# Optimization experiments

Measured on AMD Instinct MI355X. Metric: run time of the kernel, lower is better.

The kernel has to match this reference:

```python
import jax, jax.numpy as jnp
import numpy as np

B, N, C, H, NC = 8, 4096, 512, 256, 1000
GRID = 64  # N = GRID*GRID unique positions
LN_EPS = 1e-5


def setup_inputs() -> dict:
    key = jax.random.key(0)
    ks = jax.random.split(key, 10)
    # unique integer grid positions, same for every batch element (original order)
    i = jnp.arange(N)
    base = jnp.stack([i % GRID, i // GRID], axis=-1).astype(jnp.float32)  # [N,2]
    pos_org = jnp.broadcast_to(base, (B, N, 2))
    # per-batch random permutation -> shuffled positions (as the backbone would emit)
    perm = jax.vmap(lambda k: jax.random.permutation(k, N))(jax.random.split(ks[0], B))  # [B,N]
    pos_shuffled = jnp.take_along_axis(pos_org, perm[..., None], axis=1)
    s = 0.02
    return {
        "feat": jax.random.normal(ks[1], (B, N, C), jnp.float32),
        "prev_out": jax.random.normal(ks[2], (B, N, C), jnp.float32),
        "pos_org": pos_org,
        "pos_shuffled": pos_shuffled,
        "proj_W": jax.random.normal(ks[3], (C, C), jnp.float32) * s,
        "proj_b": jnp.zeros((C,), jnp.float32),
        "ln_g": jnp.ones((C,), jnp.float32),
        "ln_b": jnp.zeros((C,), jnp.float32),
        "W1": jax.random.normal(ks[4], (H, C), jnp.float32) * s,
        "b1": jnp.zeros((H,), jnp.float32),
        "W2": jax.random.normal(ks[5], (H, H), jnp.float32) * s,
        "b2": jnp.zeros((H,), jnp.float32),
        "W3": jax.random.normal(ks[6], (NC, H), jnp.float32) * s,
        "b3": jnp.zeros((NC,), jnp.float32),
    }


def _layernorm(x, g, b):
    x32 = x.astype(jnp.float32)
    mu = x32.mean(-1, keepdims=True)
    var = ((x32 - mu) ** 2).mean(-1, keepdims=True)
    return (x32 - mu) * jax.lax.rsqrt(var + LN_EPS) * g + b


def reference(feat, prev_out, pos_org, pos_shuffled, proj_W, proj_b,
              ln_g, ln_b, W1, b1, W2, b2, W3, b3):
    # find_pos_org_order: L1 cdist [B,N,N] + argmin over shuffled axis
    dists = jnp.abs(pos_org[:, :, None, :] - pos_shuffled[:, None, :, :]).sum(-1)
    pos_indices = jnp.argmin(dists, axis=2)  # [B,N]
    # batched gather: feat[b_, pos_indices]
    g = jnp.take_along_axis(feat, pos_indices[..., None], axis=1)  # [B,N,C]
    # fused proj -> layernorm (in fp32) -> cast back -> residual add
    proj = jnp.einsum('bnc,dc->bnd', g, proj_W) + proj_b
    out_feat = prev_out + _layernorm(proj, ln_g, ln_b).astype(feat.dtype)
    # mean-pool over tokens, 3-layer MLP head with relu on first two layers
    pooled = out_feat.mean(1)  # [B,C]
    h = jax.nn.relu(pooled @ W1.T + b1)
    h = jax.nn.relu(h @ W2.T + b2)
    return h @ W3.T + b3  # [B, num_classes]
```

## Files before the change

### kernel.cpp

```cpp
#include <hip/hip_runtime.h>
#include <stdint.h>

#define B_ 8
#define N_ 4096
#define C_ 512
#define H_ 256
#define NC_ 1000

typedef float v4f __attribute__((ext_vector_type(4)));
typedef short v8s __attribute__((ext_vector_type(8)));
typedef unsigned short ushort_t;

__device__ __forceinline__ uint32_t f2bf1(float f) {
    uint32_t u = __float_as_uint(f);
    return (u + 0x7FFFu + ((u >> 16) & 1u)) >> 16;
}
__device__ __forceinline__ uint32_t f2bf2(float lo, float hi) {
    return f2bf1(lo) | (f2bf1(hi) << 16);
}

__global__ void prep_kernel(const float* __restrict__ ps, const float* __restrict__ W,
                            int* __restrict__ inv, ushort_t* __restrict__ Wfrag) {
    int blk = blockIdx.x, t = threadIdx.x;
    if (blk < 128) {
        int gid = blk * 256 + t;
        float2 p = ((const float2*)ps)[gid];
        int key = (int)(p.x + 0.5f) + 64 * (int)(p.y + 0.5f);
        int b = gid >> 12;
        inv[(b << 12) + key] = gid & 4095;
    } else {
        int i = (blk - 128) * 256 + t;
        int d = i >> 6, kb = (i >> 2) & 15, q = i & 3;
        const float4* src = (const float4*)(W + d * C_ + kb * 32 + q * 8);
        float4 v0 = src[0], v1 = src[1];
        uint4 pk;
        pk.x = f2bf2(v0.x, v0.y); pk.y = f2bf2(v0.z, v0.w);
        pk.z = f2bf2(v1.x, v1.y); pk.w = f2bf2(v1.z, v1.w);
        ((uint4*)Wfrag)[((d >> 4) * 16 + kb) * 64 + q * 16 + (d & 15)] = pk;
    }
}

__global__ __launch_bounds__(512, 4)
void gemm_ln_pool(const float* __restrict__ feat, const float* __restrict__ prev,
                  const int* __restrict__ inv, const ushort_t* __restrict__ Wfrag,
                  const float* __restrict__ pb, const float* __restrict__ lg,
                  const float* __restrict__ lb, float* __restrict__ pooled) {
    __shared__ v8s Abuf[512];
    __shared__ float RowS[64], RowQ[64], ColS[512];

    const int t = threadIdx.x;
    const int b = blockIdx.x >> 6;
    const int row0 = (blockIdx.x & 63) << 6;
    const int wv = t >> 6, lane = t & 63, c = lane & 15, q = lane >> 4;

    if (t < 64) { RowS[t] = 0.f; RowQ[t] = 0.f; }

    const int arow = t >> 3;
    const int kcl = (t & 7) ^ (arow & 7);
    const int grow = inv[(b << 12) + row0 + arow];
    const float* asrc = feat + ((b * N_ + grow) * C_) + kcl * 8;

    const float* psrc = prev + ((b * N_ + row0) * C_) + t;
    float prevsum = 0.f;

    const ushort_t* fb[4];
#pragma unroll
    for (int nt = 0; nt < 4; nt++)
        fb[nt] = Wfrag + (wv * 4 + nt) * 8192 + lane * 8;

    v4f acc[4][4];
    const v4f vzero = {0.f, 0.f, 0.f, 0.f};
#pragma unroll
    for (int mt = 0; mt < 4; mt++)
#pragma unroll
        for (int nt = 0; nt < 4; nt++) acc[mt][nt] = vzero;

    for (int it = 0; it < 8; it++) {
        float4 f0 = ((const float4*)(asrc + it * 64))[0];
        float4 f1 = ((const float4*)(asrc + it * 64))[1];
#pragma unroll
        for (int rr = 0; rr < 8; rr++) prevsum += psrc[(it * 8 + rr) * C_];
        uint4 pk;
        pk.x = f2bf2(f0.x, f0.y); pk.y = f2bf2(f0.z, f0.w);
        pk.z = f2bf2(f1.x, f1.y); pk.w = f2bf2(f1.z, f1.w);
        ((uint4*)Abuf)[t] = pk;
        __syncthreads();

#pragma unroll
        for (int kk = 0; kk < 2; kk++) {
            const int kb = it * 2 + kk;
            v8s af[4], bf[4];
            const int ph = (kk * 4 + q) ^ (c & 7);
#pragma unroll
            for (int mt = 0; mt < 4; mt++) af[mt] = Abuf[mt * 128 + c * 8 + ph];
#pragma unroll
            for (int nt = 0; nt < 4; nt++)
                bf[nt] = *((const v8s*)(fb[nt] + kb * 512));
#pragma unroll
            for (int mt = 0; mt < 4; mt++)
#pragma unroll
                for (int nt = 0; nt < 4; nt++)
                    acc[mt][nt] = __builtin_amdgcn_mfma_f32_16x16x32_bf16(
                        af[mt], bf[nt], acc[mt][nt], 0, 0, 0);
        }
        __syncthreads();
    }

    float pb4[4], lg4[4], lb4[4];
#pragma unroll
    for (int nt = 0; nt < 4; nt++) {
        int n = wv * 64 + nt * 16 + c;
        pb4[nt] = pb[n]; lg4[nt] = lg[n]; lb4[nt] = lb[n];
    }
#pragma unroll
    for (int mt = 0; mt < 4; mt++) {
#pragma unroll
        for (int reg = 0; reg < 4; reg++) {
            float s1 = 0.f, s2 = 0.f;
#pragma unroll
            for (int nt = 0; nt < 4; nt++) {
                float v = acc[mt][nt][reg] + pb4[nt];
                acc[mt][nt][reg] = v;
                s1 += v; s2 += v * v;
            }
#pragma unroll
            for (int d = 1; d < 16; d <<= 1) {
                s1 += __shfl_xor(s1, d);
                s2 += __shfl_xor(s2, d);
            }
            if (c == 0) {
                int r = mt * 16 + q * 4 + reg;
                atomicAdd(&RowS[r], s1);
                atomicAdd(&RowQ[r], s2);
            }
        }
    }
    __syncthreads();
    if (t < 64) {
        float mu = RowS[t] * (1.f / C_);
        float var = RowQ[t] * (1.f / C_) - mu * mu;
        RowS[t] = mu;
        RowQ[t] = rsqrtf(var + 1e-5f);
    }
    __syncthreads();
    float col[4] = {0.f, 0.f, 0.f, 0.f};
#pragma unroll
    for (int mt = 0; mt < 4; mt++) {
#pragma unroll
        for (int reg = 0; reg < 4; reg++) {
            int r = mt * 16 + q * 4 + reg;
            float mu = RowS[r], rs = RowQ[r];
#pragma unroll
            for (int nt = 0; nt < 4; nt++)
                col[nt] += (acc[mt][nt][reg] - mu) * rs * lg4[nt] + lb4[nt];
        }
    }
#pragma unroll
    for (int nt = 0; nt < 4; nt++) {
        col[nt] += __shfl_xor(col[nt], 16);
        col[nt] += __shfl_xor(col[nt], 32);
    }
    if (lane < 16) {
#pragma unroll
        for (int nt = 0; nt < 4; nt++) ColS[wv * 64 + nt * 16 + c] = col[nt];
    }
    __syncthreads();
    atomicAdd(&pooled[b * C_ + t], ColS[t] + prevsum);
}

__global__ __launch_bounds__(256)
void head1(const float* __restrict__ pooled, const float* __restrict__ W1,
           const float* __restrict__ b1, float* __restrict__ h1) {
    const int t = threadIdx.x, wv = t >> 6, lane = t & 63;
    const int b = blockIdx.x >> 6;
    const int j = ((blockIdx.x & 63) << 2) + wv;
    const float4* wr = (const float4*)(W1 + j * C_);
    const float4* pr = (const float4*)(pooled + b * C_);
    float4 w0 = wr[lane], w1 = wr[lane + 64];
    float4 p0 = pr[lane], p1 = pr[lane + 64];
    float s = w0.x * p0.x + w0.y * p0.y + w0.z * p0.z + w0.w * p0.w
            + w1.x * p1.x + w1.y * p1.y + w1.z * p1.z + w1.w * p1.w;
#pragma unroll
    for (int d = 1; d < 64; d <<= 1) s += __shfl_xor(s, d);
    if (lane == 0) h1[b * H_ + j] = fmaxf(s * (1.f / 4096.f) + b1[j], 0.f);
}

__global__ __launch_bounds__(256)
void head2(const float* __restrict__ h1, const float* __restrict__ W2,
           const float* __restrict__ b2, float* __restrict__ h2) {
    const int t = threadIdx.x, wv = t >> 6, lane = t & 63;
    const int b = blockIdx.x >> 6;
    const int j = ((blockIdx.x & 63) << 2) + wv;
    float4 w0 = ((const float4*)(W2 + j * H_))[lane];
    float4 p0 = ((const float4*)(h1 + b * H_))[lane];
    float s = w0.x * p0.x + w0.y * p0.y + w0.z * p0.z + w0.w * p0.w;
#pragma unroll
    for (int d = 1; d < 64; d <<= 1) s += __shfl_xor(s, d);
    if (lane == 0) h2[b * H_ + j] = fmaxf(s + b2[j], 0.f);
}

__global__ __launch_bounds__(256)
void head3(const float* __restrict__ h2, const float* __restrict__ W3,
           const float* __restrict__ b3, float* __restrict__ out) {
    const int t = threadIdx.x, wv = t >> 6, lane = t & 63;
    const int b = blockIdx.x / 250;
    const int o = (blockIdx.x % 250) * 4 + wv;
    float4 w0 = ((const float4*)(W3 + o * H_))[lane];
    float4 p0 = ((const float4*)(h2 + b * H_))[lane];
    float s = w0.x * p0.x + w0.y * p0.y + w0.z * p0.z + w0.w * p0.w;
#pragma unroll
    for (int d = 1; d < 64; d <<= 1) s += __shfl_xor(s, d);
    if (lane == 0) out[b * NC_ + o] = s + b3[o];
}

extern "C" void kernel_launch(void* const* d_in, const int* in_sizes, int n_in,
                              void* d_out, int out_size, void* d_ws, size_t ws_size,
                              hipStream_t stream) {
    const float* feat  = (const float*)d_in[0];
    const float* prev  = (const float*)d_in[1];
    const float* ps    = (const float*)d_in[3];
    const float* projW = (const float*)d_in[4];
    const float* pb    = (const float*)d_in[5];
    const float* lg    = (const float*)d_in[6];
    const float* lb    = (const float*)d_in[7];
    const float* W1    = (const float*)d_in[8];
    const float* b1    = (const float*)d_in[9];
    const float* W2    = (const float*)d_in[10];
    const float* b2    = (const float*)d_in[11];
    const float* W3    = (const float*)d_in[12];
    const float* b3    = (const float*)d_in[13];
    float* out = (float*)d_out;

    char* ws = (char*)d_ws;
    ushort_t* Wfrag = (ushort_t*)ws;
    int* inv        = (int*)(ws + 524288);
    float* pooled   = (float*)(ws + 655360);
    float* h1       = (float*)(ws + 671744);
    float* h2       = (float*)(ws + 679936);

    hipMemsetAsync(pooled, 0, B_ * C_ * sizeof(float), stream);
    prep_kernel<<<256, 256, 0, stream>>>(ps, projW, inv, Wfrag);
    gemm_ln_pool<<<512, 512, 0, stream>>>(feat, prev, inv, Wfrag,
                                          pb, lg, lb, pooled);
    head1<<<512, 256, 0, stream>>>(pooled, W1, b1, h1);
    head2<<<512, 256, 0, stream>>>(h1, W2, b2, h2);
    head3<<<2000, 256, 0, stream>>>(h2, W3, b3, out);
}
```

Baseline: 241.7 us.

## Stage full A tile in LDS upfront, row-per-wave gather, fold memset into prep

The gemm kernel now gathers all 64 permuted feature rows into a 64KB LDS buffer before the MFMA loop. Each wave loads whole contiguous rows, which gives coalesced 2KB reads, and the prev row-sum loads are batched. This removes the per-iteration __syncthreads pairs and interleaved small loads, but the larger LDS footprint reduces how many blocks fit per CU. The pooled zeroing is also moved from a separate hipMemsetAsync into prep_kernel to drop one launch.

```diff
diff --git a/kernel.cpp b/kernel.cpp
--- a/kernel.cpp
+++ b/kernel.cpp
@@ -20,8 +20,14 @@
 }
 
 __global__ void prep_kernel(const float* __restrict__ ps, const float* __restrict__ W,
-                            int* __restrict__ inv, ushort_t* __restrict__ Wfrag) {
+                            int* __restrict__ inv, ushort_t* __restrict__ Wfrag,
+                            float* __restrict__ pooled) {
     int blk = blockIdx.x, t = threadIdx.x;
+    if (blk == 0) {
+        float4 z = {0.f, 0.f, 0.f, 0.f};
+#pragma unroll
+        for (int i = 0; i < 4; i++) ((float4*)pooled)[t * 4 + i] = z;
+    }
     if (blk < 128) {
         int gid = blk * 256 + t;
         float2 p = ((const float2*)ps)[gid];
@@ -45,7 +51,7 @@
                   const int* __restrict__ inv, const ushort_t* __restrict__ Wfrag,
                   const float* __restrict__ pb, const float* __restrict__ lg,
                   const float* __restrict__ lb, float* __restrict__ pooled) {
-    __shared__ v8s Abuf[512];
+    __shared__ v8s Abuf[4096];
     __shared__ float RowS[64], RowQ[64], ColS[512];
 
     const int t = threadIdx.x;
@@ -55,55 +61,63 @@
 
     if (t < 64) { RowS[t] = 0.f; RowQ[t] = 0.f; }
 
-    const int arow = t >> 3;
-    const int kcl = (t & 7) ^ (arow & 7);
-    const int grow = inv[(b << 12) + row0 + arow];
-    const float* asrc = feat + ((b * N_ + grow) * C_) + kcl * 8;
-
-    const float* psrc = prev + ((b * N_ + row0) * C_) + t;
-    float prevsum = 0.f;
-
-    const ushort_t* fb[4];
-#pragma unroll
-    for (int nt = 0; nt < 4; nt++)
-        fb[nt] = Wfrag + (wv * 4 + nt) * 8192 + lane * 8;
-
-    v4f acc[4][4];
-    const v4f vzero = {0.f, 0.f, 0.f, 0.f};
-#pragma unroll
-    for (int mt = 0; mt < 4; mt++)
-#pragma unroll
-        for (int nt = 0; nt < 4; nt++) acc[mt][nt] = vzero;
-
-    for (int it = 0; it < 8; it++) {
-        float4 f0 = ((const float4*)(asrc + it * 64))[0];
-        float4 f1 = ((const float4*)(asrc + it * 64))[1];
-#pragma unroll
-        for (int rr = 0; rr < 8; rr++) prevsum += psrc[(it * 8 + rr) * C_];
+    const int ch = lane;
+    int gr[8];
+#pragma unroll
+    for (int s = 0; s < 8; s++)
+        gr[s] = inv[(b << 12) + row0 + s * 8 + wv];
+
+#pragma unroll 2
+    for (int s = 0; s < 8; s++) {
+        const float4* src = ((const float4*)(feat + ((size_t)(b * N_ + gr[s]) * C_))) + ch * 2;
+        float4 f0 = src[0], f1 = src[1];
         uint4 pk;
         pk.x = f2bf2(f0.x, f0.y); pk.y = f2bf2(f0.z, f0.w);
         pk.z = f2bf2(f1.x, f1.y); pk.w = f2bf2(f1.z, f1.w);
-        ((uint4*)Abuf)[t] = pk;
-        __syncthreads();
-
-#pragma unroll
-        for (int kk = 0; kk < 2; kk++) {
-            const int kb = it * 2 + kk;
-            v8s af[4], bf[4];
-            const int ph = (kk * 4 + q) ^ (c & 7);
-#pragma unroll
-            for (int mt = 0; mt < 4; mt++) af[mt] = Abuf[mt * 128 + c * 8 + ph];
+        const int r = s * 8 + wv;
+        ((uint4*)Abuf)[r * 64 + (ch ^ wv)] = pk;
+    }
+
+    const float* psrc = prev + ((b * N_ + row0) * C_) + t;
+    float prevsum = 0.f;
+#pragma unroll
+    for (int g = 0; g < 8; g++) {
+        float tmp[8];
+#pragma unroll
+        for (int r = 0; r < 8; r++) tmp[r] = psrc[(g * 8 + r) * C_];
+#pragma unroll
+        for (int r = 0; r < 8; r++) prevsum += tmp[r];
+    }
+
+    const ushort_t* fb[4];
+#pragma unroll
+    for (int nt = 0; nt < 4; nt++)
+        fb[nt] = Wfrag + (wv * 4 + nt) * 8192 + lane * 8;
+
+    v4f acc[4][4];
+    const v4f vzero = {0.f, 0.f, 0.f, 0.f};
+#pragma unroll
+    for (int mt = 0; mt < 4; mt++)
+#pragma unroll
+        for (int nt = 0; nt < 4; nt++) acc[mt][nt] = vzero;
+
+    __syncthreads();
+
+#pragma unroll 2
+    for (int kb = 0; kb < 16; kb++) {
+        v8s af[4], bf[4];
+#pragma unroll
+        for (int nt = 0; nt < 4; nt++)
+            bf[nt] = *((const v8s*)(fb[nt] + kb * 512));
+#pragma unroll
+        for (int mt = 0; mt < 4; mt++)
+            af[mt] = Abuf[(mt * 16 + c) * 64 + ((kb * 4 + q) ^ (c & 7))];
+#pragma unroll
+        for (int mt = 0; mt < 4; mt++)
 #pragma unroll
             for (int nt = 0; nt < 4; nt++)
-                bf[nt] = *((const v8s*)(fb[nt] + kb * 512));
-#pragma unroll
-            for (int mt = 0; mt < 4; mt++)
-#pragma unroll
-                for (int nt = 0; nt < 4; nt++)
-                    acc[mt][nt] = __builtin_amdgcn_mfma_f32_16x16x32_bf16(
-                        af[mt], bf[nt], acc[mt][nt], 0, 0, 0);
-        }
-        __syncthreads();
+                acc[mt][nt] = __builtin_amdgcn_mfma_f32_16x16x32_bf16(
+                    af[mt], bf[nt], acc[mt][nt], 0, 0, 0);
     }
 
     float pb4[4], lg4[4], lb4[4];
@@ -238,8 +252,7 @@
     float* h1       = (float*)(ws + 671744);
     float* h2       = (float*)(ws + 679936);
 
-    hipMemsetAsync(pooled, 0, B_ * C_ * sizeof(float), stream);
-    prep_kernel<<<256, 256, 0, stream>>>(ps, projW, inv, Wfrag);
+    prep_kernel<<<256, 256, 0, stream>>>(ps, projW, inv, Wfrag, pooled);
     gemm_ln_pool<<<512, 512, 0, stream>>>(feat, prev, inv, Wfrag,
                                           pb, lg, lb, pooled);
     head1<<<512, 256, 0, stream>>>(pooled, W1, b1, h1);
```

Result: faster. 236.0 us (-2.4%).
